# Kernel tuning notes

Hardware: AMD Instinct MI355X
Metric: run time of the kernel (lower is better)

Reference implementation:

```python
import jax, jax.numpy as jnp
import numpy as np

B, T, N, F = 4, 24, 4096, 128
DIM, DIM_ATTN, RANK, HEAD = 128, 128, 32, 4
HEAD_DIM = DIM_ATTN // HEAD


def setup_inputs() -> dict:
    key = jax.random.key(0)
    ks = jax.random.split(key, 6)
    x = jax.random.normal(ks[0], (B, T, N, F), dtype=jnp.float32)
    # nn.Linear(dim, dim_attn): weight (out, in), bias (out,)
    Wq = jax.random.normal(ks[1], (DIM_ATTN, DIM), dtype=jnp.float32) / np.sqrt(DIM)
    bq = jnp.zeros((DIM_ATTN,), dtype=jnp.float32)
    # low-rank key parameter (rank, head, head_dim)
    key_param = jax.random.normal(ks[2], (RANK, HEAD, HEAD_DIM), dtype=jnp.float32)
    # nn.Linear(dim, dim)
    Wv = jax.random.normal(ks[3], (DIM, DIM), dtype=jnp.float32) / np.sqrt(DIM)
    bv = jnp.zeros((DIM,), dtype=jnp.float32)
    alpha = jnp.full((HEAD, 1), np.log(9.0), dtype=jnp.float32)
    beta = jnp.full((HEAD, 1), np.log(0.01), dtype=jnp.float32)
    return {"x": x, "Wq": Wq, "bq": bq, "key_param": key_param,
            "Wv": Wv, "bv": bv, "alpha": alpha, "beta": beta}


def reference(x, Wq, bq, key_param, Wv, bv, alpha, beta):
    b, t, n, f = x.shape
    q = (x @ Wq.T + bq).reshape(b, t, n, HEAD, HEAD_DIM)
    # scores over the rank dimension
    attn = jnp.einsum('btnhd,rhd->btnhr', q, key_param) / np.sqrt(HEAD_DIM)
    xv = (x @ Wv.T + bv).reshape(b, t, n, HEAD, HEAD_DIM)
    # stage 1: softmax over rank (last axis), aggregate values into rank slots
    v = jnp.einsum('btnhr,btnhd->btrhd', jax.nn.softmax(attn, axis=-1), xv)
    # stage 2: softmax over nodes (axis -3 == n), redistribute to nodes
    v = jnp.einsum('btnhr,btrhd->btnhd', jax.nn.softmax(attn, axis=-3), v)
    # sigmoid-gated residual mix; alpha/beta (head,1) broadcast over d
    v = jax.nn.sigmoid(alpha) * xv + jax.nn.sigmoid(beta) * v
    return v.reshape(b, t, n, f)
```

## Files before the change

### kernel.cpp

```cpp
#include <hip/hip_runtime.h>

constexpr int Nn = 4096, Fc = 128;
constexpr int Rr = 32, Hh = 4, Dd = 32;
constexpr int BT = 96;
constexpr float SCALE = 0.17677669529663687f;

constexpr size_t OFF_V1  = 0;
constexpr size_t OFF_Z   = (size_t)BT * Hh * Rr * Dd;
constexpr size_t OFF_BQK = OFF_Z + (size_t)BT * Hh * Rr;
constexpr size_t OFF_U   = OFF_BQK + 128;

constexpr int U_WKHI = 0, U_WVHI = 16384, U_WVLO = 32768;

using short8  = __attribute__((ext_vector_type(8))) short;
using floatx4 = __attribute__((ext_vector_type(4))) float;

__device__ inline ushort f2bf(float f) {
    union { float f; unsigned u; } c{f};
    unsigned r = c.u + 0x7fffu + ((c.u >> 16) & 1u);
    return (ushort)(r >> 16);
}
__device__ inline float bf2f(ushort u) {
    union { unsigned u; float f; } c{(unsigned)u << 16};
    return c.f;
}

__global__ void kprep(const float* __restrict__ Wq, const float* __restrict__ bq,
                      const float* __restrict__ Wv, const float* __restrict__ key,
                      ushort* __restrict__ U, float* __restrict__ bqk)
{
    const int idx = blockIdx.x * 256 + threadIdx.x;
    if (idx < 16384) {
        const int hr = idx >> 7, f = idx & 127;
        const int h = hr >> 5, r = hr & 31;
        float s = 0.f;
#pragma unroll
        for (int d = 0; d < 32; d++)
            s += Wq[(h * 32 + d) * 128 + f] * key[(r * 4 + h) * 32 + d];
        U[U_WKHI + idx] = f2bf(s);
    } else if (idx < 32768) {
        const int o = idx - 16384;
        const float v = Wv[o];
        const ushort h = f2bf(v);
        U[U_WVHI + o] = h;
        U[U_WVLO + o] = f2bf(v - bf2f(h));
    } else if (idx < 32768 + 128) {
        const int hr = idx - 32768;
        const int h = hr >> 5, r = hr & 31;
        float s = 0.f;
#pragma unroll
        for (int d = 0; d < 32; d++)
            s += bq[h * 32 + d] * key[(r * 4 + h) * 32 + d];
        bqk[hr] = s;
    }
}

__global__ __launch_bounds__(256, 2)
void ka(const float* __restrict__ x, const float* __restrict__ bv,
        const ushort* __restrict__ U, const float* __restrict__ bqk,
        float* __restrict__ v1, float* __restrict__ Z)
{
    __shared__ __align__(16) char lds[71680];

    const int t = threadIdx.x;
    const int w = t >> 6, lane = t & 63;
    const int quad = lane >> 4, l15 = lane & 15;
    const int bt = blockIdx.y;
    constexpr int NT = 4;

    char* wsc = lds + 34816 + w * 9216;
    ushort* eT  = (ushort*)wsc;
    ushort* xvT = (ushort*)(wsc + 4608);

    const ushort* WKh = U + U_WKHI;
    const ushort* Wvh = U + U_WVHI;

    float bvv[2], bqkv[2];
#pragma unroll
    for (int i = 0; i < 2; i++) {
        bvv[i]  = bv[32 * w + 16 * i + l15];
        bqkv[i] = bqk[32 * w + 16 * i + l15];
    }

    floatx4 accV1[2][2];
#pragma unroll
    for (int i = 0; i < 2; i++)
#pragma unroll
        for (int j = 0; j < 2; j++) accV1[i][j] = (floatx4)0.f;
    float zacc[2] = {0.f, 0.f};

    const float* xbase = x + ((size_t)bt * Nn + blockIdx.x * (NT * 64)) * Fc;

    float4 xr[8];
#pragma unroll
    for (int i = 0; i < 8; i++) xr[i] = ((const float4*)xbase)[i * 256 + t];

#pragma unroll 1
    for (int it = 0; it < NT; ++it) {
        ushort* xh = (ushort*)(lds + (it & 1) * 17408);
#pragma unroll
        for (int i = 0; i < 8; i++) {
            const int idx = i * 256 + t;
            const int row = idx >> 5, c4 = idx & 31;
            float4 v = xr[i];
            ushort4 hv;
            hv.x = f2bf(v.x); hv.y = f2bf(v.y); hv.z = f2bf(v.z); hv.w = f2bf(v.w);
            *(ushort4*)&xh[row * 136 + c4 * 4] = hv;
        }
        __syncthreads();

        floatx4 acca[4][2], accv[4][2];
#pragma unroll
        for (int mt = 0; mt < 4; mt++)
#pragma unroll
            for (int nt = 0; nt < 2; nt++) {
                acca[mt][nt] = (floatx4)0.f;
                accv[mt][nt] = (floatx4)0.f;
            }

#pragma unroll
        for (int kc = 0; kc < 4; kc++) {
            short8 ah[4];
#pragma unroll
            for (int mt = 0; mt < 4; mt++)
                ah[mt] = *(const short8*)&xh[(16 * mt + l15) * 136 + kc * 32 + quad * 8];
            short8 kb2[2], vb[2];
#pragma unroll
            for (int nt = 0; nt < 2; nt++) {
                const int off = (32 * w + 16 * nt + l15) * 128 + kc * 32 + quad * 8;
                kb2[nt] = *(const short8*)&WKh[off];
                vb[nt]  = *(const short8*)&Wvh[off];
            }
#pragma unroll
            for (int mt = 0; mt < 4; mt++)
#pragma unroll
                for (int nt = 0; nt < 2; nt++) {
                    acca[mt][nt] = __builtin_amdgcn_mfma_f32_16x16x32_bf16(ah[mt], kb2[nt], acca[mt][nt], 0, 0, 0);
                    accv[mt][nt] = __builtin_amdgcn_mfma_f32_16x16x32_bf16(ah[mt], vb[nt],  accv[mt][nt], 0, 0, 0);
                }
        }

        if (it + 1 < NT) {
            const float4* xg = (const float4*)(xbase + (size_t)(it + 1) * 64 * Fc);
#pragma unroll
            for (int i = 0; i < 8; i++) xr[i] = xg[i * 256 + t];
        }

        float sloc[4][4];
#pragma unroll
        for (int mt = 0; mt < 4; mt++)
#pragma unroll
            for (int reg = 0; reg < 4; reg++) {
                const int n = 16 * mt + 4 * quad + reg;
                const float e0 = __expf((acca[mt][0][reg] + bqkv[0]) * SCALE);
                const float e1 = __expf((acca[mt][1][reg] + bqkv[1]) * SCALE);
                eT[l15 * 72 + n]        = f2bf(e0);
                eT[(16 + l15) * 72 + n] = f2bf(e1);
                zacc[0] += e0; zacc[1] += e1;
                sloc[mt][reg] = e0 + e1;
            }
#pragma unroll
        for (int m = 1; m < 16; m <<= 1)
#pragma unroll
            for (int mt = 0; mt < 4; mt++)
#pragma unroll
                for (int reg = 0; reg < 4; reg++)
                    sloc[mt][reg] += __shfl_xor(sloc[mt][reg], m);

#pragma unroll
        for (int mt = 0; mt < 4; mt++)
#pragma unroll
            for (int reg = 0; reg < 4; reg++) {
                const int n = 16 * mt + 4 * quad + reg;
                const float sw = 1.f / sloc[mt][reg];
#pragma unroll
                for (int nt = 0; nt < 2; nt++)
                    xvT[(16 * nt + l15) * 72 + n] =
                        f2bf((accv[mt][nt][reg] + bvv[nt]) * sw);
            }

#pragma unroll
        for (int kn = 0; kn < 2; kn++) {
            short8 ae[2], bx[2];
#pragma unroll
            for (int i = 0; i < 2; i++) {
                ae[i] = *(const short8*)&eT[(16 * i + l15) * 72 + kn * 32 + quad * 8];
                bx[i] = *(const short8*)&xvT[(16 * i + l15) * 72 + kn * 32 + quad * 8];
            }
#pragma unroll
            for (int mt = 0; mt < 2; mt++)
#pragma unroll
                for (int nt = 0; nt < 2; nt++)
                    accV1[mt][nt] = __builtin_amdgcn_mfma_f32_16x16x32_bf16(ae[mt], bx[nt], accV1[mt][nt], 0, 0, 0);
        }
    }

#pragma unroll
    for (int rt = 0; rt < 2; rt++) {
        float zr = zacc[rt];
        zr += __shfl_xor(zr, 16);
        zr += __shfl_xor(zr, 32);
        if (quad == 0)
            atomicAdd(&Z[((size_t)bt * Hh + w) * Rr + 16 * rt + l15], zr);
    }
    float* v1b = v1 + ((size_t)bt * Hh + w) * Rr * Dd;
#pragma unroll
    for (int mt = 0; mt < 2; mt++)
#pragma unroll
        for (int nt = 0; nt < 2; nt++)
#pragma unroll
            for (int reg = 0; reg < 4; reg++)
                atomicAdd(&v1b[(16 * mt + 4 * quad + reg) * 32 + 16 * nt + l15],
                          accV1[mt][nt][reg]);
}

__global__ __launch_bounds__(256, 2)
void kb(const float* __restrict__ x, const float* __restrict__ bv,
        const ushort* __restrict__ U, const float* __restrict__ bqk,
        const float* __restrict__ v1, const float* __restrict__ Z,
        const float* __restrict__ alpha, const float* __restrict__ beta,
        float* __restrict__ out)
{
    __shared__ __align__(16) char lds[53248];
    ushort* xhi = (ushort*)lds;
    ushort* xlo = (ushort*)(lds + 17408);

    const int t = threadIdx.x;
    const int w = t >> 6, lane = t & 63;
    const int quad = lane >> 4, l15 = lane & 15;
    const int bt = blockIdx.y;
    constexpr int NT = 4;

    char* wsc = lds + 34816 + w * 4608;
    ushort* eS = (ushort*)wsc;
    float*  fS = (float*)wsc;

    const ushort* WKh = U + U_WKHI;
    const ushort* Wvh = U + U_WVHI;
    const ushort* Wvl = U + U_WVLO;

    float bqkv[2], bvv[2];
#pragma unroll
    for (int i = 0; i < 2; i++) {
        bqkv[i] = bqk[32 * w + 16 * i + l15];
        bvv[i]  = bv[32 * w + 16 * i + l15];
    }

    const float* v1h = v1 + ((size_t)bt * Hh + w) * Rr * Dd;
    const float* Zh  = Z + ((size_t)bt * Hh + w) * Rr;
    float zr8[8];
#pragma unroll
    for (int j = 0; j < 8; j++) zr8[j] = 1.f / Zh[8 * quad + j];
    short8 vbz[2];
#pragma unroll
    for (int dt = 0; dt < 2; dt++) {
        union { short8 s; unsigned u[4]; } uu;
#pragma unroll
        for (int jj = 0; jj < 4; jj++) {
            const float a0 = v1h[(8 * quad + 2 * jj) * 32 + 16 * dt + l15] * zr8[2 * jj];
            const float a1 = v1h[(8 * quad + 2 * jj + 1) * 32 + 16 * dt + l15] * zr8[2 * jj + 1];
            uu.u[jj] = ((unsigned)f2bf(a1) << 16) | f2bf(a0);
        }
        vbz[dt] = uu.s;
    }
    const float sa = 1.f / (1.f + __expf(-alpha[w]));
    const float sb = 1.f / (1.f + __expf(-beta[w]));

    const float* xbase = x + ((size_t)bt * Nn + blockIdx.x * (NT * 64)) * Fc;
    float* obase = out + ((size_t)bt * Nn + blockIdx.x * (NT * 64)) * Fc;

    float4 xr[8];
#pragma unroll
    for (int i = 0; i < 8; i++) xr[i] = ((const float4*)xbase)[i * 256 + t];

#pragma unroll 1
    for (int it = 0; it < NT; ++it) {
#pragma unroll
        for (int i = 0; i < 8; i++) {
            const int idx = i * 256 + t;
            const int row = idx >> 5, c4 = idx & 31;
            float4 v = xr[i];
            ushort h0 = f2bf(v.x), h1 = f2bf(v.y), h2 = f2bf(v.z), h3 = f2bf(v.w);
            ushort4 hv; hv.x = h0; hv.y = h1; hv.z = h2; hv.w = h3;
            ushort4 lv; lv.x = f2bf(v.x - bf2f(h0)); lv.y = f2bf(v.y - bf2f(h1));
            lv.z = f2bf(v.z - bf2f(h2)); lv.w = f2bf(v.w - bf2f(h3));
            *(ushort4*)&xhi[row * 136 + c4 * 4] = hv;
            *(ushort4*)&xlo[row * 136 + c4 * 4] = lv;
        }
        __syncthreads();

        floatx4 acca[4][2], accv[4][2];
#pragma unroll
        for (int mt = 0; mt < 4; mt++)
#pragma unroll
            for (int nt = 0; nt < 2; nt++) {
                acca[mt][nt] = (floatx4)0.f;
                accv[mt][nt] = (floatx4)0.f;
            }

#pragma unroll
        for (int kc = 0; kc < 4; kc++) {
            short8 ahi[4], alo[4];
#pragma unroll
            for (int mt = 0; mt < 4; mt++) {
                const int ro = (16 * mt + l15) * 136 + kc * 32 + quad * 8;
                ahi[mt] = *(const short8*)&xhi[ro];
                alo[mt] = *(const short8*)&xlo[ro];
            }
            short8 kb2[2], vbh[2], vbl[2];
#pragma unroll
            for (int nt = 0; nt < 2; nt++) {
                const int off = (32 * w + 16 * nt + l15) * 128 + kc * 32 + quad * 8;
                kb2[nt] = *(const short8*)&WKh[off];
                vbh[nt] = *(const short8*)&Wvh[off];
                vbl[nt] = *(const short8*)&Wvl[off];
            }
#pragma unroll
            for (int mt = 0; mt < 4; mt++)
#pragma unroll
                for (int nt = 0; nt < 2; nt++) {
                    acca[mt][nt] = __builtin_amdgcn_mfma_f32_16x16x32_bf16(ahi[mt], kb2[nt], acca[mt][nt], 0, 0, 0);
                    accv[mt][nt] = __builtin_amdgcn_mfma_f32_16x16x32_bf16(ahi[mt], vbh[nt], accv[mt][nt], 0, 0, 0);
                    accv[mt][nt] = __builtin_amdgcn_mfma_f32_16x16x32_bf16(ahi[mt], vbl[nt], accv[mt][nt], 0, 0, 0);
                    accv[mt][nt] = __builtin_amdgcn_mfma_f32_16x16x32_bf16(alo[mt], vbh[nt], accv[mt][nt], 0, 0, 0);
                }
        }
        __syncthreads();

        if (it + 1 < NT) {
            const float4* xg = (const float4*)(xbase + (size_t)(it + 1) * 64 * Fc);
#pragma unroll
            for (int i = 0; i < 8; i++) xr[i] = xg[i * 256 + t];
        }

        float* op = obase + (size_t)it * 64 * Fc;

#pragma unroll
        for (int half = 0; half < 2; half++) {
#pragma unroll
            for (int mtl = 0; mtl < 2; mtl++) {
                const int mt = 2 * half + mtl;
#pragma unroll
                for (int rt = 0; rt < 2; rt++)
#pragma unroll
                    for (int reg = 0; reg < 4; reg++) {
                        const int row = 16 * mtl + 4 * quad + reg;
                        eS[row * 40 + 16 * rt + l15] =
                            f2bf(__expf((acca[mt][rt][reg] + bqkv[rt]) * SCALE));
                    }
            }
            floatx4 acc2[2][2];
#pragma unroll
            for (int mtl = 0; mtl < 2; mtl++) {
                short8 pa = *(const short8*)&eS[(16 * mtl + l15) * 40 + quad * 8];
#pragma unroll
                for (int dt = 0; dt < 2; dt++) {
                    acc2[mtl][dt] = (floatx4)0.f;
                    acc2[mtl][dt] = __builtin_amdgcn_mfma_f32_16x16x32_bf16(pa, vbz[dt], acc2[mtl][dt], 0, 0, 0);
                }
            }
#pragma unroll
            for (int mtl = 0; mtl < 2; mtl++) {
                const int mt = 2 * half + mtl;
#pragma unroll
                for (int nt = 0; nt < 2; nt++)
#pragma unroll
                    for (int reg = 0; reg < 4; reg++) {
                        const int row = 16 * mtl + 4 * quad + reg;
                        fS[row * 36 + 16 * nt + l15] =
                            sa * (accv[mt][nt][reg] + bvv[nt]) + sb * acc2[mtl][nt][reg];
                    }
            }
#pragma unroll
            for (int i = 0; i < 4; i++) {
                const int idx = i * 64 + lane;
                const int n = idx >> 3, c4 = idx & 7;
                *(float4*)&op[(size_t)(32 * half + n) * 128 + w * 32 + c4 * 4] =
                    *(const float4*)&fS[n * 36 + c4 * 4];
            }
        }
    }
}

extern "C" void kernel_launch(void* const* d_in, const int* in_sizes, int n_in,
                              void* d_out, int out_size, void* d_ws, size_t ws_size,
                              hipStream_t stream)
{
    const float* x     = (const float*)d_in[0];
    const float* Wq    = (const float*)d_in[1];
    const float* bq    = (const float*)d_in[2];
    const float* key   = (const float*)d_in[3];
    const float* Wv    = (const float*)d_in[4];
    const float* bv    = (const float*)d_in[5];
    const float* alpha = (const float*)d_in[6];
    const float* beta  = (const float*)d_in[7];
    float* out = (float*)d_out;

    float*  ws   = (float*)d_ws;
    float*  v1   = ws + OFF_V1;
    float*  Zb   = ws + OFF_Z;
    float*  bqkp = ws + OFF_BQK;
    ushort* U    = (ushort*)(ws + OFF_U);

    hipMemsetAsync(v1, 0,
                   (size_t)(BT * Hh * Rr * Dd + BT * Hh * Rr) * sizeof(float),
                   stream);
    kprep<<<dim3(129), 256, 0, stream>>>(Wq, bq, Wv, key, U, bqkp);
    ka<<<dim3(16, BT), 256, 0, stream>>>(x, bv, U, bqkp, v1, Zb);
    kb<<<dim3(16, BT), 256, 0, stream>>>(x, bv, U, bqkp, v1, Zb, alpha, beta, out);
}
```

Measured before the change: 486.8 us.

## Split each block's rows across 8 waves with 512-thread blocks

Both kernels now launch 512 threads per block. Eight waves split the work by head and by half of the 64-row tile, so each wave holds half as many accumulators and x staging registers. The goal is more resident waves per CU to hide global-load and MFMA latency in what looks like a latency-bound streaming kernel. In exchange, weight fragments are loaded twice per block, ka issues twice as many v1/Z atomics, and per-block LDS grows.

```diff
diff --git a/kernel.cpp b/kernel.cpp
--- a/kernel.cpp
+++ b/kernel.cpp
@@ -55,22 +55,23 @@
     }
 }
 
-__global__ __launch_bounds__(256, 2)
+__global__ __launch_bounds__(512, 4)
 void ka(const float* __restrict__ x, const float* __restrict__ bv,
         const ushort* __restrict__ U, const float* __restrict__ bqk,
         float* __restrict__ v1, float* __restrict__ Z)
 {
-    __shared__ __align__(16) char lds[71680];
+    __shared__ __align__(16) char lds[75776];
 
     const int t = threadIdx.x;
     const int w = t >> 6, lane = t & 63;
+    const int h = w & 3, half = w >> 2;
     const int quad = lane >> 4, l15 = lane & 15;
     const int bt = blockIdx.y;
     constexpr int NT = 4;
 
-    char* wsc = lds + 34816 + w * 9216;
+    char* wsc = lds + 34816 + w * 5120;
     ushort* eT  = (ushort*)wsc;
-    ushort* xvT = (ushort*)(wsc + 4608);
+    ushort* xvT = (ushort*)(wsc + 2560);
 
     const ushort* WKh = U + U_WKHI;
     const ushort* Wvh = U + U_WVHI;
@@ -78,8 +79,8 @@
     float bvv[2], bqkv[2];
 #pragma unroll
     for (int i = 0; i < 2; i++) {
-        bvv[i]  = bv[32 * w + 16 * i + l15];
-        bqkv[i] = bqk[32 * w + 16 * i + l15];
+        bvv[i]  = bv[32 * h + 16 * i + l15];
+        bqkv[i] = bqk[32 * h + 16 * i + l15];
     }
 
     floatx4 accV1[2][2];
@@ -91,16 +92,16 @@
 
     const float* xbase = x + ((size_t)bt * Nn + blockIdx.x * (NT * 64)) * Fc;
 
-    float4 xr[8];
-#pragma unroll
-    for (int i = 0; i < 8; i++) xr[i] = ((const float4*)xbase)[i * 256 + t];
+    float4 xr[4];
+#pragma unroll
+    for (int i = 0; i < 4; i++) xr[i] = ((const float4*)xbase)[i * 512 + t];
 
 #pragma unroll 1
     for (int it = 0; it < NT; ++it) {
         ushort* xh = (ushort*)(lds + (it & 1) * 17408);
 #pragma unroll
-        for (int i = 0; i < 8; i++) {
-            const int idx = i * 256 + t;
+        for (int i = 0; i < 4; i++) {
+            const int idx = i * 512 + t;
             const int row = idx >> 5, c4 = idx & 31;
             float4 v = xr[i];
             ushort4 hv;
@@ -109,9 +110,9 @@
         }
         __syncthreads();
 
-        floatx4 acca[4][2], accv[4][2];
-#pragma unroll
-        for (int mt = 0; mt < 4; mt++)
+        floatx4 acca[2][2], accv[2][2];
+#pragma unroll
+        for (int mt = 0; mt < 2; mt++)
 #pragma unroll
             for (int nt = 0; nt < 2; nt++) {
                 acca[mt][nt] = (floatx4)0.f;
@@ -120,19 +121,19 @@
 
 #pragma unroll
         for (int kc = 0; kc < 4; kc++) {
-            short8 ah[4];
-#pragma unroll
-            for (int mt = 0; mt < 4; mt++)
-                ah[mt] = *(const short8*)&xh[(16 * mt + l15) * 136 + kc * 32 + quad * 8];
+            short8 ah[2];
+#pragma unroll
+            for (int mt = 0; mt < 2; mt++)
+                ah[mt] = *(const short8*)&xh[(32 * half + 16 * mt + l15) * 136 + kc * 32 + quad * 8];
             short8 kb2[2], vb[2];
 #pragma unroll
             for (int nt = 0; nt < 2; nt++) {
-                const int off = (32 * w + 16 * nt + l15) * 128 + kc * 32 + quad * 8;
+                const int off = (32 * h + 16 * nt + l15) * 128 + kc * 32 + quad * 8;
                 kb2[nt] = *(const short8*)&WKh[off];
                 vb[nt]  = *(const short8*)&Wvh[off];
             }
 #pragma unroll
-            for (int mt = 0; mt < 4; mt++)
+            for (int mt = 0; mt < 2; mt++)
 #pragma unroll
                 for (int nt = 0; nt < 2; nt++) {
                     acca[mt][nt] = __builtin_amdgcn_mfma_f32_16x16x32_bf16(ah[mt], kb2[nt], acca[mt][nt], 0, 0, 0);
@@ -143,49 +144,48 @@
         if (it + 1 < NT) {
             const float4* xg = (const float4*)(xbase + (size_t)(it + 1) * 64 * Fc);
 #pragma unroll
-            for (int i = 0; i < 8; i++) xr[i] = xg[i * 256 + t];
-        }
-
-        float sloc[4][4];
-#pragma unroll
-        for (int mt = 0; mt < 4; mt++)
+            for (int i = 0; i < 4; i++) xr[i] = xg[i * 512 + t];
+        }
+
+        float sloc[2][4];
+#pragma unroll
+        for (int mt = 0; mt < 2; mt++)
 #pragma unroll
             for (int reg = 0; reg < 4; reg++) {
-                const int n = 16 * mt + 4 * quad + reg;
+                const int nl = 16 * mt + 4 * quad + reg;
                 const float e0 = __expf((acca[mt][0][reg] + bqkv[0]) * SCALE);
                 const float e1 = __expf((acca[mt][1][reg] + bqkv[1]) * SCALE);
-                eT[l15 * 72 + n]        = f2bf(e0);
-                eT[(16 + l15) * 72 + n] = f2bf(e1);
+                eT[l15 * 40 + nl]        = f2bf(e0);
+                eT[(16 + l15) * 40 + nl] = f2bf(e1);
                 zacc[0] += e0; zacc[1] += e1;
                 sloc[mt][reg] = e0 + e1;
             }
 #pragma unroll
         for (int m = 1; m < 16; m <<= 1)
 #pragma unroll
-            for (int mt = 0; mt < 4; mt++)
+            for (int mt = 0; mt < 2; mt++)
 #pragma unroll
                 for (int reg = 0; reg < 4; reg++)
                     sloc[mt][reg] += __shfl_xor(sloc[mt][reg], m);
 
 #pragma unroll
-        for (int mt = 0; mt < 4; mt++)
+        for (int mt = 0; mt < 2; mt++)
 #pragma unroll
             for (int reg = 0; reg < 4; reg++) {
-                const int n = 16 * mt + 4 * quad + reg;
+                const int nl = 16 * mt + 4 * quad + reg;
                 const float sw = 1.f / sloc[mt][reg];
 #pragma unroll
                 for (int nt = 0; nt < 2; nt++)
-                    xvT[(16 * nt + l15) * 72 + n] =
+                    xvT[(16 * nt + l15) * 40 + nl] =
                         f2bf((accv[mt][nt][reg] + bvv[nt]) * sw);
             }
 
-#pragma unroll
-        for (int kn = 0; kn < 2; kn++) {
+        {
             short8 ae[2], bx[2];
 #pragma unroll
             for (int i = 0; i < 2; i++) {
-                ae[i] = *(const short8*)&eT[(16 * i + l15) * 72 + kn * 32 + quad * 8];
-                bx[i] = *(const short8*)&xvT[(16 * i + l15) * 72 + kn * 32 + quad * 8];
+                ae[i] = *(const short8*)&eT[(16 * i + l15) * 40 + quad * 8];
+                bx[i] = *(const short8*)&xvT[(16 * i + l15) * 40 + quad * 8];
             }
 #pragma unroll
             for (int mt = 0; mt < 2; mt++)
@@ -201,9 +201,9 @@
         zr += __shfl_xor(zr, 16);
         zr += __shfl_xor(zr, 32);
         if (quad == 0)
-            atomicAdd(&Z[((size_t)bt * Hh + w) * Rr + 16 * rt + l15], zr);
-    }
-    float* v1b = v1 + ((size_t)bt * Hh + w) * Rr * Dd;
+            atomicAdd(&Z[((size_t)bt * Hh + h) * Rr + 16 * rt + l15], zr);
+    }
+    float* v1b = v1 + ((size_t)bt * Hh + h) * Rr * Dd;
 #pragma unroll
     for (int mt = 0; mt < 2; mt++)
 #pragma unroll
@@ -214,19 +214,20 @@
                           accV1[mt][nt][reg]);
 }
 
-__global__ __launch_bounds__(256, 2)
+__global__ __launch_bounds__(512, 4)
 void kb(const float* __restrict__ x, const float* __restrict__ bv,
         const ushort* __restrict__ U, const float* __restrict__ bqk,
         const float* __restrict__ v1, const float* __restrict__ Z,
         const float* __restrict__ alpha, const float* __restrict__ beta,
         float* __restrict__ out)
 {
-    __shared__ __align__(16) char lds[53248];
+    __shared__ __align__(16) char lds[71680];
     ushort* xhi = (ushort*)lds;
     ushort* xlo = (ushort*)(lds + 17408);
 
     const int t = threadIdx.x;
     const int w = t >> 6, lane = t & 63;
+    const int h = w & 3, half = w >> 2;
     const int quad = lane >> 4, l15 = lane & 15;
     const int bt = blockIdx.y;
     constexpr int NT = 4;
@@ -242,12 +243,12 @@
     float bqkv[2], bvv[2];
 #pragma unroll
     for (int i = 0; i < 2; i++) {
-        bqkv[i] = bqk[32 * w + 16 * i + l15];
-        bvv[i]  = bv[32 * w + 16 * i + l15];
-    }
-
-    const float* v1h = v1 + ((size_t)bt * Hh + w) * Rr * Dd;
-    const float* Zh  = Z + ((size_t)bt * Hh + w) * Rr;
+        bqkv[i] = bqk[32 * h + 16 * i + l15];
+        bvv[i]  = bv[32 * h + 16 * i + l15];
+    }
+
+    const float* v1h = v1 + ((size_t)bt * Hh + h) * Rr * Dd;
+    const float* Zh  = Z + ((size_t)bt * Hh + h) * Rr;
     float zr8[8];
 #pragma unroll
     for (int j = 0; j < 8; j++) zr8[j] = 1.f / Zh[8 * quad + j];
@@ -263,21 +264,21 @@
         }
         vbz[dt] = uu.s;
     }
-    const float sa = 1.f / (1.f + __expf(-alpha[w]));
-    const float sb = 1.f / (1.f + __expf(-beta[w]));
+    const float sa = 1.f / (1.f + __expf(-alpha[h]));
+    const float sb = 1.f / (1.f + __expf(-beta[h]));
 
     const float* xbase = x + ((size_t)bt * Nn + blockIdx.x * (NT * 64)) * Fc;
     float* obase = out + ((size_t)bt * Nn + blockIdx.x * (NT * 64)) * Fc;
 
-    float4 xr[8];
-#pragma unroll
-    for (int i = 0; i < 8; i++) xr[i] = ((const float4*)xbase)[i * 256 + t];
+    float4 xr[4];
+#pragma unroll
+    for (int i = 0; i < 4; i++) xr[i] = ((const float4*)xbase)[i * 512 + t];
 
 #pragma unroll 1
     for (int it = 0; it < NT; ++it) {
 #pragma unroll
-        for (int i = 0; i < 8; i++) {
-            const int idx = i * 256 + t;
+        for (int i = 0; i < 4; i++) {
+            const int idx = i * 512 + t;
             const int row = idx >> 5, c4 = idx & 31;
             float4 v = xr[i];
             ushort h0 = f2bf(v.x), h1 = f2bf(v.y), h2 = f2bf(v.z), h3 = f2bf(v.w);
@@ -289,9 +290,9 @@
         }
         __syncthreads();
 
-        floatx4 acca[4][2], accv[4][2];
-#pragma unroll
-        for (int mt = 0; mt < 4; mt++)
+        floatx4 acca[2][2], accv[2][2];
+#pragma unroll
+        for (int mt = 0; mt < 2; mt++)
 #pragma unroll
             for (int nt = 0; nt < 2; nt++) {
                 acca[mt][nt] = (floatx4)0.f;
@@ -300,23 +301,23 @@
 
 #pragma unroll
         for (int kc = 0; kc < 4; kc++) {
-            short8 ahi[4], alo[4];
-#pragma unroll
-            for (int mt = 0; mt < 4; mt++) {
-                const int ro = (16 * mt + l15) * 136 + kc * 32 + quad * 8;
+            short8 ahi[2], alo[2];
+#pragma unroll
+            for (int mt = 0; mt < 2; mt++) {
+                const int ro = (32 * half + 16 * mt + l15) * 136 + kc * 32 + quad * 8;
                 ahi[mt] = *(const short8*)&xhi[ro];
                 alo[mt] = *(const short8*)&xlo[ro];
             }
             short8 kb2[2], vbh[2], vbl[2];
 #pragma unroll
             for (int nt = 0; nt < 2; nt++) {
-                const int off = (32 * w + 16 * nt + l15) * 128 + kc * 32 + quad * 8;
+                const int off = (32 * h + 16 * nt + l15) * 128 + kc * 32 + quad * 8;
                 kb2[nt] = *(const short8*)&WKh[off];
                 vbh[nt] = *(const short8*)&Wvh[off];
                 vbl[nt] = *(const short8*)&Wvl[off];
             }
 #pragma unroll
-            for (int mt = 0; mt < 4; mt++)
+            for (int mt = 0; mt < 2; mt++)
 #pragma unroll
                 for (int nt = 0; nt < 2; nt++) {
                     acca[mt][nt] = __builtin_amdgcn_mfma_f32_16x16x32_bf16(ahi[mt], kb2[nt], acca[mt][nt], 0, 0, 0);
@@ -330,54 +331,46 @@
         if (it + 1 < NT) {
             const float4* xg = (const float4*)(xbase + (size_t)(it + 1) * 64 * Fc);
 #pragma unroll
-            for (int i = 0; i < 8; i++) xr[i] = xg[i * 256 + t];
-        }
-
+            for (int i = 0; i < 4; i++) xr[i] = xg[i * 512 + t];
+        }
+
+#pragma unroll
+        for (int mt = 0; mt < 2; mt++)
+#pragma unroll
+            for (int rt = 0; rt < 2; rt++)
+#pragma unroll
+                for (int reg = 0; reg < 4; reg++) {
+                    const int row = 16 * mt + 4 * quad + reg;
+                    eS[row * 40 + 16 * rt + l15] =
+                        f2bf(__expf((acca[mt][rt][reg] + bqkv[rt]) * SCALE));
+                }
+        floatx4 acc2[2][2];
+#pragma unroll
+        for (int mt = 0; mt < 2; mt++) {
+            short8 pa = *(const short8*)&eS[(16 * mt + l15) * 40 + quad * 8];
+#pragma unroll
+            for (int dt = 0; dt < 2; dt++) {
+                acc2[mt][dt] = (floatx4)0.f;
+                acc2[mt][dt] = __builtin_amdgcn_mfma_f32_16x16x32_bf16(pa, vbz[dt], acc2[mt][dt], 0, 0, 0);
+            }
+        }
+#pragma unroll
+        for (int mt = 0; mt < 2; mt++)
+#pragma unroll
+            for (int nt = 0; nt < 2; nt++)
+#pragma unroll
+                for (int reg = 0; reg < 4; reg++) {
+                    const int row = 16 * mt + 4 * quad + reg;
+                    fS[row * 36 + 16 * nt + l15] =
+                        sa * (accv[mt][nt][reg] + bvv[nt]) + sb * acc2[mt][nt][reg];
+                }
         float* op = obase + (size_t)it * 64 * Fc;
-
-#pragma unroll
-        for (int half = 0; half < 2; half++) {
-#pragma unroll
-            for (int mtl = 0; mtl < 2; mtl++) {
-                const int mt = 2 * half + mtl;
-#pragma unroll
-                for (int rt = 0; rt < 2; rt++)
-#pragma unroll
-                    for (int reg = 0; reg < 4; reg++) {
-                        const int row = 16 * mtl + 4 * quad + reg;
-                        eS[row * 40 + 16 * rt + l15] =
-                            f2bf(__expf((acca[mt][rt][reg] + bqkv[rt]) * SCALE));
-                    }
-            }
-            floatx4 acc2[2][2];
-#pragma unroll
-            for (int mtl = 0; mtl < 2; mtl++) {
-                short8 pa = *(const short8*)&eS[(16 * mtl + l15) * 40 + quad * 8];
-#pragma unroll
-                for (int dt = 0; dt < 2; dt++) {
-                    acc2[mtl][dt] = (floatx4)0.f;
-                    acc2[mtl][dt] = __builtin_amdgcn_mfma_f32_16x16x32_bf16(pa, vbz[dt], acc2[mtl][dt], 0, 0, 0);
-                }
-            }
-#pragma unroll
-            for (int mtl = 0; mtl < 2; mtl++) {
-                const int mt = 2 * half + mtl;
-#pragma unroll
-                for (int nt = 0; nt < 2; nt++)
-#pragma unroll
-                    for (int reg = 0; reg < 4; reg++) {
-                        const int row = 16 * mtl + 4 * quad + reg;
-                        fS[row * 36 + 16 * nt + l15] =
-                            sa * (accv[mt][nt][reg] + bvv[nt]) + sb * acc2[mtl][nt][reg];
-                    }
-            }
-#pragma unroll
-            for (int i = 0; i < 4; i++) {
-                const int idx = i * 64 + lane;
-                const int n = idx >> 3, c4 = idx & 7;
-                *(float4*)&op[(size_t)(32 * half + n) * 128 + w * 32 + c4 * 4] =
-                    *(const float4*)&fS[n * 36 + c4 * 4];
-            }
+#pragma unroll
+        for (int i = 0; i < 4; i++) {
+            const int idx = i * 64 + lane;
+            const int n = idx >> 3, c4 = idx & 7;
+            *(float4*)&op[(size_t)(32 * half + n) * 128 + h * 32 + c4 * 4] =
+                *(const float4*)&fS[n * 36 + c4 * 4];
         }
     }
 }
@@ -406,6 +399,6 @@
                    (size_t)(BT * Hh * Rr * Dd + BT * Hh * Rr) * sizeof(float),
                    stream);
     kprep<<<dim3(129), 256, 0, stream>>>(Wq, bq, Wv, key, U, bqkp);
-    ka<<<dim3(16, BT), 256, 0, stream>>>(x, bv, U, bqkp, v1, Zb);
-    kb<<<dim3(16, BT), 256, 0, stream>>>(x, bv, U, bqkp, v1, Zb, alpha, beta, out);
-}
+    ka<<<dim3(16, BT), 512, 0, stream>>>(x, bv, U, bqkp, v1, Zb);
+    kb<<<dim3(16, BT), 512, 0, stream>>>(x, bv, U, bqkp, v1, Zb, alpha, beta, out);
+}
```

New measurement: 725.8 us. 1.49x slower.
